# Kernel tuning notes

Hardware: AMD Instinct MI355X
Metric: run time of the kernel (lower is better)

Reference implementation:

```python
import jax, jax.numpy as jnp
import numpy as np

B, H, S, D = 2, 16, 2048, 64

def setup_inputs() -> dict:
    key = jax.random.key(0)
    kq, kk, kv = jax.random.split(key, 3)
    q = jax.random.normal(kq, (B, H, S, D), dtype=jnp.float32)
    k = jax.random.normal(kk, (B, H, S, D), dtype=jnp.float32)
    v = jax.random.normal(kv, (B, H, S, D), dtype=jnp.float32)
    return {"q": q, "k": k, "v": v}

def reference(q, k, v):
    # Faithful to the source: raw exp (no max-subtraction), no 1/sqrt(d) scaling.
    scores = jnp.einsum("bhsd,bhtd->bhst", q, k)          # [B,H,S,S]
    scores_exp = jnp.exp(scores)
    probs = scores_exp / jnp.sum(scores_exp, axis=-1, keepdims=True)
    return jnp.einsum("bhst,bhtd->bhsd", probs, v)         # [B,H,S,D]
```

## Files before the change

kernel.cpp:

```cpp
#include <hip/hip_runtime.h>


#define LOG2E 1.44269504088896340736f

typedef _Float16 half8 __attribute__((ext_vector_type(8)));
typedef _Float16 half2v __attribute__((ext_vector_type(2)));
typedef __fp16 fp16x2 __attribute__((ext_vector_type(2)));
typedef float f32x16 __attribute__((ext_vector_type(16)));

#define BH   32
#define SEQ  2048
#define DIM  64
#define QBLK 128
#define KVB  32
#define NIT  (SEQ / (2 * KVB))

union SMem {
  struct { _Float16 K[2][KVB * DIM]; _Float16 Vt[2][DIM * KVB]; } s;
  struct { float ob[2][2][2][16 * 64]; float ml[2][2][2][64]; } c;
};

static __device__ __forceinline__ unsigned pk2(float a, float b) {
  fp16x2 h = __builtin_amdgcn_cvt_pkrtz(a, b);
  return __builtin_bit_cast(unsigned, h);
}

static __device__ __forceinline__ void plswap(unsigned& a, unsigned& b) {
  asm volatile("v_permlane32_swap_b32 %0, %1" : "+v"(a), "+v"(b));
}

static __device__ __forceinline__ float xmax32(float x) {
  return fmaxf(x, __shfl_xor(x, 32));
}
static __device__ __forceinline__ float xsum32(float x) {
  return x + __shfl_xor(x, 32);
}

static __device__ __forceinline__ float dot2(unsigned a, float acc) {
  const half2v ones = {(_Float16)1.0f, (_Float16)1.0f};
  return __builtin_amdgcn_fdot2(__builtin_bit_cast(half2v, a), ones, acc, false);
}

__launch_bounds__(256, 2)
__global__ void attn_fwd(const float* __restrict__ Q, const float* __restrict__ K,
                         const float* __restrict__ V, float* __restrict__ O) {
  __shared__ __align__(16) SMem sm;

  const int tid  = threadIdx.x;
  const int lane = tid & 63;
  const int wave = tid >> 6;
  const int wq   = wave & 1;
  const int wk   = wave >> 1;
  const int hi   = lane >> 5;
  const int lq   = lane & 31;

  const int bid  = blockIdx.x;
  const int xcd  = bid & 7;
  const int slot = bid >> 3;
  const int bh   = xcd + 8 * (slot >> 4);
  const int qt   = slot & 15;

  const size_t base = (size_t)bh * SEQ * DIM;
  const int qr0 = qt * QBLK + wq * 64 + lq;
  const float* qpA = Q + base + (size_t)qr0 * DIM;
  const float* qpB = qpA + 32 * DIM;

  half8 qfA[4], qfB[4];
#pragma unroll
  for (int c = 0; c < 4; ++c) {
    float4 a0 = *(const float4*)(qpA + 16 * c + 8 * hi);
    float4 a1 = *(const float4*)(qpA + 16 * c + 8 * hi + 4);
    union { unsigned u[4]; half8 v; } h;
    h.u[0] = pk2(a0.x, a0.y); h.u[1] = pk2(a0.z, a0.w);
    h.u[2] = pk2(a1.x, a1.y); h.u[3] = pk2(a1.z, a1.w);
    qfA[c] = h.v;
    float4 b0 = *(const float4*)(qpB + 16 * c + 8 * hi);
    float4 b1 = *(const float4*)(qpB + 16 * c + 8 * hi + 4);
    h.u[0] = pk2(b0.x, b0.y); h.u[1] = pk2(b0.z, b0.w);
    h.u[2] = pk2(b1.x, b1.y); h.u[3] = pk2(b1.z, b1.w);
    qfB[c] = h.v;
  }

  f32x16 oA0 = {}, oA1 = {}, oB0 = {}, oB1 = {};
  float mA = -1e30f, lA = 0.f, mB = -1e30f, lB = 0.f;

  float4 kreg[2][2];
  float  vreg[2][8];
  const int kr  = tid >> 3;
  const int kd  = (tid & 7) * 8;
  const int vd  = tid & 63;
  const int vk0 = (tid >> 6) * 8;
  const float* kbp = K + base;
  const float* vbp = V + base;

  auto LOADT = [&](int it) {
#pragma unroll
    for (int p = 0; p < 2; ++p) {
      const int t = 2 * it + p;
      const float* kp = kbp + (size_t)(t * KVB + kr) * DIM + kd;
      kreg[p][0] = *(const float4*)(kp);
      kreg[p][1] = *(const float4*)(kp + 4);
      const float* vp = vbp + (size_t)(t * KVB + vk0) * DIM + vd;
#pragma unroll
      for (int j = 0; j < 8; ++j) vreg[p][j] = vp[j * DIM];
    }
  };

  auto STORET = [&]() {
#pragma unroll
    for (int p = 0; p < 2; ++p) {
      union { unsigned u[4]; half8 v; } h;
      h.u[0] = pk2(kreg[p][0].x, kreg[p][0].y);
      h.u[1] = pk2(kreg[p][0].z, kreg[p][0].w);
      h.u[2] = pk2(kreg[p][1].x, kreg[p][1].y);
      h.u[3] = pk2(kreg[p][1].z, kreg[p][1].w);
      const int idx = (kr * DIM + kd) ^ ((kr & 7) << 3);
      *(half8*)&sm.s.K[p][idx] = h.v;
      union { unsigned u[4]; half8 v; } g;
      g.u[0] = pk2(vreg[p][0], vreg[p][1]);
      g.u[1] = pk2(vreg[p][2], vreg[p][3]);
      g.u[2] = pk2(vreg[p][4], vreg[p][5]);
      g.u[3] = pk2(vreg[p][6], vreg[p][7]);
      const int vidx = (vd * KVB + vk0) ^ ((vd & 7) << 3);
      *(half8*)&sm.s.Vt[p][vidx] = g.v;
    }
  };

  auto softmax_set = [&](const f32x16& s, float& m, float& l,
                         f32x16& o0, f32x16& o1, half8& pv0, half8& pv1) {
    float t0 = fmaxf(fmaxf(s[0],  s[1]),  s[2]);
    float t1 = fmaxf(fmaxf(s[3],  s[4]),  s[5]);
    float t2 = fmaxf(fmaxf(s[6],  s[7]),  s[8]);
    float t3 = fmaxf(fmaxf(s[9],  s[10]), s[11]);
    float t4 = fmaxf(fmaxf(s[12], s[13]), s[14]);
    float t5 = fmaxf(fmaxf(t0, t1), t2);
    float t6 = fmaxf(fmaxf(t3, t4), s[15]);
    float t  = xmax32(fmaxf(t5, t6));
    if (__any(t > m + 10.f)) {
      const float mn = fmaxf(m, t);
      const float corr = __builtin_amdgcn_exp2f((m - mn) * LOG2E);
      m = mn; l *= corr;
#pragma unroll
      for (int i = 0; i < 16; ++i) { o0[i] *= corr; o1[i] *= corr; }
    }
    const float nml2 = -m * LOG2E;
    float p[16];
#pragma unroll
    for (int i = 0; i < 16; ++i)
      p[i] = __builtin_amdgcn_exp2f(__builtin_fmaf(s[i], LOG2E, nml2));

    unsigned w[8];
#pragma unroll
    for (int i = 0; i < 8; ++i) w[i] = pk2(p[2 * i], p[2 * i + 1]);

    float la = dot2(w[0], 0.f), lb2 = dot2(w[1], 0.f);
    la = dot2(w[2], la); lb2 = dot2(w[3], lb2);
    la = dot2(w[4], la); lb2 = dot2(w[5], lb2);
    la = dot2(w[6], la); lb2 = dot2(w[7], lb2);
    l += la + lb2;

    plswap(w[0], w[2]); plswap(w[1], w[3]);
    plswap(w[4], w[6]); plswap(w[5], w[7]);
    union { unsigned u[4]; half8 v; } f;
    f.u[0] = w[0]; f.u[1] = w[1]; f.u[2] = w[2]; f.u[3] = w[3];
    pv0 = f.v;
    f.u[0] = w[4]; f.u[1] = w[5]; f.u[2] = w[6]; f.u[3] = w[7];
    pv1 = f.v;
  };

  LOADT(0);
  for (int it = 0; it < NIT; ++it) {
    __syncthreads();
    STORET();
    if (it + 1 < NIT) LOADT(it + 1);
    __syncthreads();

    const _Float16* Kt = sm.s.K[wk];
    const _Float16* Vt = sm.s.Vt[wk];

    const int ksw = (lq & 7) << 3;
    f32x16 sA = {}, sB = {};
    __builtin_amdgcn_s_setprio(1);
#pragma unroll
    for (int c = 0; c < 4; ++c) {
      half8 a = *(const half8*)&Kt[(lq * DIM + c * 16 + hi * 8) ^ ksw];
      sA = __builtin_amdgcn_mfma_f32_32x32x16_f16(a, qfA[c], sA, 0, 0, 0);
      sB = __builtin_amdgcn_mfma_f32_32x32x16_f16(a, qfB[c], sB, 0, 0, 0);
    }
    __builtin_amdgcn_s_setprio(0);

    half8 pA0, pA1, pB0, pB1;
    softmax_set(sA, mA, lA, oA0, oA1, pA0, pA1);
    softmax_set(sB, mB, lB, oB0, oB1, pB0, pB1);

    const int d0 = lq, d1 = 32 + lq;
    const int sz0 = (d0 & 7) << 3, sz1 = (d1 & 7) << 3;
    __builtin_amdgcn_s_setprio(1);
    {
      half8 a = *(const half8*)&Vt[(d0 * KVB + 0 + hi * 8) ^ sz0];
      oA0 = __builtin_amdgcn_mfma_f32_32x32x16_f16(a, pA0, oA0, 0, 0, 0);
      oB0 = __builtin_amdgcn_mfma_f32_32x32x16_f16(a, pB0, oB0, 0, 0, 0);
    }
    {
      half8 a = *(const half8*)&Vt[(d1 * KVB + 0 + hi * 8) ^ sz1];
      oA1 = __builtin_amdgcn_mfma_f32_32x32x16_f16(a, pA0, oA1, 0, 0, 0);
      oB1 = __builtin_amdgcn_mfma_f32_32x32x16_f16(a, pB0, oB1, 0, 0, 0);
    }
    {
      half8 a = *(const half8*)&Vt[(d0 * KVB + 16 + hi * 8) ^ sz0];
      oA0 = __builtin_amdgcn_mfma_f32_32x32x16_f16(a, pA1, oA0, 0, 0, 0);
      oB0 = __builtin_amdgcn_mfma_f32_32x32x16_f16(a, pB1, oB0, 0, 0, 0);
    }
    {
      half8 a = *(const half8*)&Vt[(d1 * KVB + 16 + hi * 8) ^ sz1];
      oA1 = __builtin_amdgcn_mfma_f32_32x32x16_f16(a, pA1, oA1, 0, 0, 0);
      oB1 = __builtin_amdgcn_mfma_f32_32x32x16_f16(a, pB1, oB1, 0, 0, 0);
    }
    __builtin_amdgcn_s_setprio(0);
  }

  lA = xsum32(lA);
  lB = xsum32(lB);

  __syncthreads();
  if (wk == 1) {
#pragma unroll
    for (int r = 0; r < 16; ++r) {
      sm.c.ob[wq][0][0][r * 64 + lane] = oA0[r];
      sm.c.ob[wq][0][1][r * 64 + lane] = oA1[r];
      sm.c.ob[wq][1][0][r * 64 + lane] = oB0[r];
      sm.c.ob[wq][1][1][r * 64 + lane] = oB1[r];
    }
    sm.c.ml[wq][0][0][lane] = mA; sm.c.ml[wq][0][1][lane] = lA;
    sm.c.ml[wq][1][0][lane] = mB; sm.c.ml[wq][1][1][lane] = lB;
  }
  __syncthreads();
  if (wk == 0) {
    auto emit = [&](int set, int qrow, const f32x16& o0, const f32x16& o1,
                    float m, float l) {
      const float mb = sm.c.ml[wq][set][0][lane];
      const float lb = sm.c.ml[wq][set][1][lane];
      const float mx = fmaxf(m, mb);
      const float ca = __builtin_amdgcn_exp2f((m - mx) * LOG2E);
      const float cb = __builtin_amdgcn_exp2f((mb - mx) * LOG2E);
      const float inv = 1.0f / (l * ca + lb * cb);
      float* op = O + base + (size_t)qrow * DIM;
#pragma unroll
      for (int g = 0; g < 4; ++g) {
        float4 r0, r1;
        r0.x = (o0[4*g+0] * ca + sm.c.ob[wq][set][0][(4*g+0)*64 + lane] * cb) * inv;
        r0.y = (o0[4*g+1] * ca + sm.c.ob[wq][set][0][(4*g+1)*64 + lane] * cb) * inv;
        r0.z = (o0[4*g+2] * ca + sm.c.ob[wq][set][0][(4*g+2)*64 + lane] * cb) * inv;
        r0.w = (o0[4*g+3] * ca + sm.c.ob[wq][set][0][(4*g+3)*64 + lane] * cb) * inv;
        r1.x = (o1[4*g+0] * ca + sm.c.ob[wq][set][1][(4*g+0)*64 + lane] * cb) * inv;
        r1.y = (o1[4*g+1] * ca + sm.c.ob[wq][set][1][(4*g+1)*64 + lane] * cb) * inv;
        r1.z = (o1[4*g+2] * ca + sm.c.ob[wq][set][1][(4*g+2)*64 + lane] * cb) * inv;
        r1.w = (o1[4*g+3] * ca + sm.c.ob[wq][set][1][(4*g+3)*64 + lane] * cb) * inv;
        *(float4*)(op + 8 * g + 4 * hi) = r0;
        *(float4*)(op + 32 + 8 * g + 4 * hi) = r1;
      }
    };
    emit(0, qr0,      oA0, oA1, mA, lA);
    emit(1, qr0 + 32, oB0, oB1, mB, lB);
  }
}

extern "C" void kernel_launch(void* const* d_in, const int* in_sizes, int n_in,
                              void* d_out, int out_size, void* d_ws, size_t ws_size,
                              hipStream_t stream) {
  const float* q = (const float*)d_in[0];
  const float* k = (const float*)d_in[1];
  const float* v = (const float*)d_in[2];
  float* o = (float*)d_out;
  attn_fwd<<<BH * (SEQ / QBLK), 256, 0, stream>>>(q, k, v, o);
}
```

Before: 62.38 us.

## Load K fragments directly from global into registers, bypassing shared memory

K tiles are no longer staged through LDS. Each wave loads its own K rows from global memory straight into registers in MFMA fragment layout, converts them to fp16, and prefetches the next tile one iteration ahead. This removes the LDS writes and reads for K and halves the shared-memory footprint. The cost is more registers per thread and global loads that are less coalesced, and K is now read redundantly by waves that share a kv tile.

```diff
diff --git a/kernel.cpp b/kernel.cpp
--- a/kernel.cpp
+++ b/kernel.cpp
@@ -16,7 +16,7 @@
 #define NIT  (SEQ / (2 * KVB))
 
 union SMem {
-  struct { _Float16 K[2][KVB * DIM]; _Float16 Vt[2][DIM * KVB]; } s;
+  struct { _Float16 Vt[2][DIM * KVB]; } s;
   struct { float ob[2][2][2][16 * 64]; float ml[2][2][2][64]; } c;
 };
 
@@ -84,38 +84,45 @@
   f32x16 oA0 = {}, oA1 = {}, oB0 = {}, oB1 = {};
   float mA = -1e30f, lA = 0.f, mB = -1e30f, lB = 0.f;
 
-  float4 kreg[2][2];
-  float  vreg[2][8];
-  const int kr  = tid >> 3;
-  const int kd  = (tid & 7) * 8;
+  float4 kf[8];
+  const float* kbp = K + base + (size_t)(wk * 32 + lq) * DIM + hi * 8;
+  auto LOADK = [&](int it) {
+    const float* kp = kbp + (size_t)it * 64 * DIM;
+#pragma unroll
+    for (int c = 0; c < 4; ++c) {
+      kf[2 * c]     = *(const float4*)(kp + 16 * c);
+      kf[2 * c + 1] = *(const float4*)(kp + 16 * c + 4);
+    }
+  };
+  auto CONVK = [&](half8* kfrag) {
+#pragma unroll
+    for (int c = 0; c < 4; ++c) {
+      union { unsigned u[4]; half8 v; } h;
+      h.u[0] = pk2(kf[2 * c].x,     kf[2 * c].y);
+      h.u[1] = pk2(kf[2 * c].z,     kf[2 * c].w);
+      h.u[2] = pk2(kf[2 * c + 1].x, kf[2 * c + 1].y);
+      h.u[3] = pk2(kf[2 * c + 1].z, kf[2 * c + 1].w);
+      kfrag[c] = h.v;
+    }
+  };
+
+  float vreg[2][8];
   const int vd  = tid & 63;
   const int vk0 = (tid >> 6) * 8;
-  const float* kbp = K + base;
   const float* vbp = V + base;
 
-  auto LOADT = [&](int it) {
+  auto LOADV = [&](int it) {
 #pragma unroll
     for (int p = 0; p < 2; ++p) {
       const int t = 2 * it + p;
-      const float* kp = kbp + (size_t)(t * KVB + kr) * DIM + kd;
-      kreg[p][0] = *(const float4*)(kp);
-      kreg[p][1] = *(const float4*)(kp + 4);
       const float* vp = vbp + (size_t)(t * KVB + vk0) * DIM + vd;
 #pragma unroll
       for (int j = 0; j < 8; ++j) vreg[p][j] = vp[j * DIM];
     }
   };
-
-  auto STORET = [&]() {
+  auto STOREV = [&]() {
 #pragma unroll
     for (int p = 0; p < 2; ++p) {
-      union { unsigned u[4]; half8 v; } h;
-      h.u[0] = pk2(kreg[p][0].x, kreg[p][0].y);
-      h.u[1] = pk2(kreg[p][0].z, kreg[p][0].w);
-      h.u[2] = pk2(kreg[p][1].x, kreg[p][1].y);
-      h.u[3] = pk2(kreg[p][1].z, kreg[p][1].w);
-      const int idx = (kr * DIM + kd) ^ ((kr & 7) << 3);
-      *(half8*)&sm.s.K[p][idx] = h.v;
       union { unsigned u[4]; half8 v; } g;
       g.u[0] = pk2(vreg[p][0], vreg[p][1]);
       g.u[1] = pk2(vreg[p][2], vreg[p][3]);
@@ -168,24 +175,25 @@
     pv1 = f.v;
   };
 
-  LOADT(0);
+  LOADK(0);
+  LOADV(0);
+
   for (int it = 0; it < NIT; ++it) {
     __syncthreads();
-    STORET();
-    if (it + 1 < NIT) LOADT(it + 1);
+    STOREV();
+    if (it + 1 < NIT) LOADV(it + 1);
     __syncthreads();
 
-    const _Float16* Kt = sm.s.K[wk];
-    const _Float16* Vt = sm.s.Vt[wk];
-
-    const int ksw = (lq & 7) << 3;
+    half8 kfrag[4];
+    CONVK(kfrag);
+    if (it + 1 < NIT) LOADK(it + 1);
+
     f32x16 sA = {}, sB = {};
     __builtin_amdgcn_s_setprio(1);
 #pragma unroll
     for (int c = 0; c < 4; ++c) {
-      half8 a = *(const half8*)&Kt[(lq * DIM + c * 16 + hi * 8) ^ ksw];
-      sA = __builtin_amdgcn_mfma_f32_32x32x16_f16(a, qfA[c], sA, 0, 0, 0);
-      sB = __builtin_amdgcn_mfma_f32_32x32x16_f16(a, qfB[c], sB, 0, 0, 0);
+      sA = __builtin_amdgcn_mfma_f32_32x32x16_f16(kfrag[c], qfA[c], sA, 0, 0, 0);
+      sB = __builtin_amdgcn_mfma_f32_32x32x16_f16(kfrag[c], qfB[c], sB, 0, 0, 0);
     }
     __builtin_amdgcn_s_setprio(0);
 
@@ -193,6 +201,7 @@
     softmax_set(sA, mA, lA, oA0, oA1, pA0, pA1);
     softmax_set(sB, mB, lB, oB0, oB1, pB0, pB1);
 
+    const _Float16* Vt = sm.s.Vt[wk];
     const int d0 = lq, d1 = 32 + lq;
     const int sz0 = (d0 & 7) << 3, sz1 = (d1 & 7) << 3;
     __builtin_amdgcn_s_setprio(1);
```

Result: slower. 79.39 us (+27.3%).
